# Kernel optimization log

Hardware: AMD Instinct MI355X
Metric: run time of the kernel (lower is better)

The kernel has to match this reference:

```python
import jax, jax.numpy as jnp
import numpy as np

D = 8        # q_ndim (= dof_ndim)
HID = 200    # hidden_size
N = 16384    # batch of states
EPS = 0.1    # qdot regularizer coefficient in L()


def _lagrangian(z, Ws, bs):
    # z: (2D,) = [q, qdot]; angular_dims=() so CosSin is an identity pass-through
    v = z[D:]
    h = z
    for W, b in zip(Ws[:-1], bs[:-1]):
        h = jax.nn.softplus(h @ W + b)   # FCsoftplus blocks
    L = (h @ Ws[-1] + bs[-1])[0]          # final Linear -> scalar (Reshape(-1))
    return L + EPS * jnp.dot(v, v)


def setup_inputs():
    key = jax.random.key(0)
    ks = jax.random.split(key, 5)
    z = jax.random.normal(ks[0], (N, 2 * D), dtype=jnp.float32)
    t = jnp.zeros((), dtype=jnp.float32)

    def lin(k, fi, fo, scale):
        return (jax.random.normal(k, (fi, fo), dtype=jnp.float32)
                * jnp.float32(scale / np.sqrt(fi)))

    W0 = lin(ks[1], 2 * D, HID, 1.0)
    W1 = lin(ks[2], HID, HID, 1.0)
    W2 = lin(ks[3], HID, HID, 1.0)
    W3 = lin(ks[4], HID, 1, 0.01)  # small head keeps mass matrix M well conditioned
    b0 = jnp.zeros((HID,), jnp.float32)  # zero_bias init per FCsoftplus/Linear
    b1 = jnp.zeros((HID,), jnp.float32)
    b2 = jnp.zeros((HID,), jnp.float32)
    b3 = jnp.zeros((1,), jnp.float32)
    return dict(t=t, z=z, W0=W0, b0=b0, W1=W1, b1=b1, W2=W2, b2=b2, W3=W3, b3=b3)


def reference(t, z, W0, b0, W1, b1, W2, b2, W3, b3):
    # Euler-Lagrange dynamics (LagrangianDynamics):
    #   M a = dL/dq - (d2L/dq dv) v,  M = d2L/dv2;  dz/dt = [v, a]
    Ws = (W0, W1, W2, W3)
    bs = (b0, b1, b2, b3)
    Lfn = lambda zz: _lagrangian(zz, Ws, bs)

    def dyn_single(zi):
        g = jax.grad(Lfn)(zi)              # (2D,)  = [dL/dq, dL/dv]
        H = jax.jacfwd(jax.grad(Lfn))(zi)  # (2D,2D) Hessian of L wrt z
        v = zi[D:]
        M = H[D:, D:]                      # d(dL/dv)/dv  -> mass matrix
        C = H[D:, :D]                      # d(dL/dv)/dq
        F = g[:D] - C @ v
        a = jnp.linalg.solve(M, F)
        return jnp.concatenate([v, a])     # (2D,)

    return jax.vmap(dyn_single)(z)         # (N, 2D)
```

## Files before the change

### kernel.cpp

```cpp
#include <hip/hip_runtime.h>
#include <math.h>

#define DD 8
#define ZD 16
#define HID 200
#define EPSL 0.1f
#define BS 16
#define NTHREADS 1024
#define NKC 7
#define NMT 13
#define XSTR 216
#define CSTR 212
#define HSTR 20
#define WSTR 208
#define NTAN 8
#define NT8 8

#define KSC 1024.0f
#define SSC 64.0f
#define INV_K (1.0f/1024.0f)
#define INV_KS (1.0f/65536.0f)

typedef _Float16 half8 __attribute__((ext_vector_type(8)));
typedef _Float16 half4v __attribute__((ext_vector_type(4)));
typedef _Float16 half2v __attribute__((ext_vector_type(2)));
typedef float float4v __attribute__((ext_vector_type(4)));

#define S4 (NKC*NMT*64*8)
#define OFF_W1T 0
#define OFF_W2T (S4)
#define OFF_W1  (2*S4)
#define OFF_W2  (3*S4)
#define OFF_W0T (4*S4)
#define OFF_W0  (4*S4 + NMT*64*8)
#define WS_HALFS (4*S4 + NMT*64*8 + NKC*64*8)

__global__ void prep(const float* __restrict__ W0, const float* __restrict__ W1,
                     const float* __restrict__ W2, _Float16* __restrict__ ws)
{
    int idx = blockIdx.x * 256 + threadIdx.x;
    if (idx >= WS_HALFS) return;
    float v = 0.f;
    if (idx < 4*S4) {
        int arr = idx / S4, e = idx % S4;
        int kc = e / (NMT*64*8); int r = e % (NMT*64*8);
        int mt = r / (64*8); r %= 64*8;
        int lane = r / 8, j = r % 8;
        int m = mt*16 + (lane & 15);
        int k = kc*32 + (lane >> 4)*8 + j;
        if (m < HID && k < HID) {
            if      (arr == 0) v = W1[k*HID + m];
            else if (arr == 1) v = W2[k*HID + m];
            else if (arr == 2) v = W1[m*HID + k];
            else               v = W2[m*HID + k];
        }
    } else if (idx < OFF_W0) {
        int e = idx - OFF_W0T;
        int mt = e / (64*8); int r = e % (64*8);
        int lane = r / 8, j = r % 8;
        int m = mt*16 + (lane & 15);
        int k = (lane >> 4)*8 + j;
        if (m < HID && k < ZD) v = W0[k*HID + m];
    } else {
        int e = idx - OFF_W0;
        int kc = e / (64*8); int r = e % (64*8);
        int lane = r / 8, j = r % 8;
        int m = (lane & 15);
        int k = kc*32 + (lane >> 4)*8 + j;
        if (k < HID) v = W0[m*HID + k];
    }
    ws[idx] = (_Float16)v;
}

__device__ __forceinline__ half4v pk4(float4v a) {
    half2v lo = __builtin_bit_cast(half2v, __builtin_amdgcn_cvt_pkrtz(a.x, a.y));
    half2v hi = __builtin_bit_cast(half2v, __builtin_amdgcn_cvt_pkrtz(a.z, a.w));
    return __builtin_shufflevector(lo, hi, 0, 1, 2, 3);
}
__device__ __forceinline__ void sig_sp(float x, float& sp, float& sg) {
    float e = __expf(-fabsf(x));
    float r = 1.0f / (1.0f + e);
    sg = (x >= 0.f) ? r : (1.0f - r);
    sp = fmaxf(x, 0.f) + __logf(1.f + e);
}

template<int NTILES, int MTC>
__device__ __forceinline__ void run_mv(const half8* __restrict__ Asw,
                                       const _Float16* __restrict__ Xsrc,
                                       int mt0, int lane,
                                       float4v acc[MTC][NTILES])
{
    const int lm = lane & 15, q = lane >> 4;
    constexpr int PF = (NTILES > 1) ? 2 : NKC;
#pragma unroll
    for (int m = 0; m < MTC; ++m)
#pragma unroll
        for (int n = 0; n < NTILES; ++n)
            acc[m][n] = (float4v){0.f, 0.f, 0.f, 0.f};

    half8 a[MTC][PF];
#pragma unroll
    for (int p = 0; p < PF; ++p)
#pragma unroll
        for (int m = 0; m < MTC; ++m)
            a[m][p] = Asw[(p*NMT + mt0 + m)*64 + lane];

#pragma unroll
    for (int kc = 0; kc < NKC; ++kc) {
        half8 x[NTILES];
#pragma unroll
        for (int n = 0; n < NTILES; ++n)
            x[n] = *(const half8*)(Xsrc + (n*16 + lm)*XSTR + kc*32 + q*8);
        half8 an[MTC];
        if (kc + PF < NKC)
#pragma unroll
            for (int m = 0; m < MTC; ++m)
                an[m] = Asw[((kc+PF)*NMT + mt0 + m)*64 + lane];
#pragma unroll
        for (int m = 0; m < MTC; ++m)
#pragma unroll
            for (int n = 0; n < NTILES; ++n)
                acc[m][n] = __builtin_amdgcn_mfma_f32_16x16x32_f16(a[m][0], x[n], acc[m][n], 0, 0, 0);
#pragma unroll
        for (int m = 0; m < MTC; ++m)
#pragma unroll
            for (int p = 0; p + 1 < PF; ++p) a[m][p] = a[m][p+1];
        if (kc + PF < NKC)
#pragma unroll
            for (int m = 0; m < MTC; ++m) a[m][PF-1] = an[m];
    }
}

__global__ void __launch_bounds__(NTHREADS, 4)
lnn_main(const float* __restrict__ z,
         const float* __restrict__ W0, const float* __restrict__ b0,
         const float* __restrict__ b1, const float* __restrict__ b2,
         const float* __restrict__ W3,
         const _Float16* __restrict__ ws,
         float* __restrict__ out)
{
    __shared__ alignas(16) _Float16 Xt[128*XSTR];
    __shared__ alignas(16) _Float16 Xb[128*XSTR];
    __shared__ alignas(16) _Float16 Cf[5][16*CSTR];
    __shared__ alignas(16) _Float16 Xz[16*40];
    __shared__ alignas(16) _Float16 bsh[4*WSTR];
    __shared__ alignas(16) _Float16 w0t[NTAN*WSTR];
    __shared__ alignas(16) float gsh[16*HSTR];
    __shared__ alignas(16) float Hr[128*HSTR];

    const int tid  = threadIdx.x;
    const int wave = tid >> 6;
    const int lane = tid & 63;
    const int lm   = lane & 15;
    const int q    = lane >> 4;
    const int s0   = blockIdx.x * BS;

    const half8* W1Tsw = (const half8*)(ws + OFF_W1T);
    const half8* W2Tsw = (const half8*)(ws + OFF_W2T);
    const half8* W1sw  = (const half8*)(ws + OFF_W1);
    const half8* W2sw  = (const half8*)(ws + OFF_W2);
    const half8* W0Tsw = (const half8*)(ws + OFF_W0T);
    const half8* W0sw  = (const half8*)(ws + OFF_W0);

    if (tid < 256) {
        int s = tid >> 4, k = tid & 15;
        Xz[s*40 + k]      = (_Float16)z[(s0 + s)*ZD + k];
        Xz[s*40 + 16 + k] = (_Float16)0.f;
    }
    for (int idx = tid; idx < 128*16; idx += NTHREADS) {
        int r = idx >> 4, c = 200 + (idx & 15);
        Xt[r*XSTR + c] = (_Float16)0.f;
        Xb[r*XSTR + c] = (_Float16)0.f;
    }
    if (tid < 8) {
        Xt[16*XSTR + tid] = (_Float16)0.f;
        Xb[16*XSTR + tid] = (_Float16)0.f;
    }
    for (int idx = tid; idx < 4*WSTR; idx += NTHREADS) {
        int l = idx / WSTR, u = idx % WSTR;
        float v = 0.f;
        if (u < HID) {
            if      (l == 0) v = b0[u];
            else if (l == 1) v = b1[u];
            else if (l == 2) v = b2[u];
            else             v = KSC * W3[u];
        }
        bsh[idx] = (_Float16)v;
    }
    for (int idx = tid; idx < NTAN*WSTR; idx += NTHREADS) {
        int t = idx / WSTR, u = idx % WSTR;
        w0t[idx] = (_Float16)((u < HID) ? SSC * W0[(DD + t)*HID + u] : 0.f);
    }
    __syncthreads();

    float4v acc1[1][1];
    const int ubf = wave*16 + q*4;

    if (wave < NMT) {
        acc1[0][0] = (float4v){0.f,0.f,0.f,0.f};
        half8 xz = *(const half8*)(Xz + lm*40 + q*8);
        half8 a = W0Tsw[wave*64 + lane];
        acc1[0][0] = __builtin_amdgcn_mfma_f32_16x16x32_f16(a, xz, acc1[0][0], 0, 0, 0);
        half4v bb = *(const half4v*)(&bsh[0*WSTR + ubf]);
        float h[4], p[4];
#pragma unroll
        for (int r = 0; r < 4; ++r) {
            float av = acc1[0][0][r] + (float)bb[r];
            sig_sp(av, h[r], p[r]);
        }
        *(half4v*)(&Xt[lm*XSTR + ubf])     = pk4((float4v){h[0],h[1],h[2],h[3]});
        *(half4v*)(&Cf[0][lm*CSTR + ubf])  = pk4((float4v){p[0],p[1],p[2],p[3]});
    }
    __syncthreads();

    if (wave < NMT) {
        run_mv<1,1>(W1Tsw, Xt, wave, lane, acc1);
        half4v bb = *(const half4v*)(&bsh[1*WSTR + ubf]);
        float h[4], p[4];
#pragma unroll
        for (int r = 0; r < 4; ++r) {
            float av = acc1[0][0][r] + (float)bb[r];
            sig_sp(av, h[r], p[r]);
        }
        *(half4v*)(&Xb[lm*XSTR + ubf])    = pk4((float4v){h[0],h[1],h[2],h[3]});
        *(half4v*)(&Cf[1][lm*CSTR + ubf]) = pk4((float4v){p[0],p[1],p[2],p[3]});
    }
    __syncthreads();

    if (wave < NMT) {
        run_mv<1,1>(W2Tsw, Xb, wave, lane, acc1);
        half4v bb = *(const half4v*)(&bsh[2*WSTR + ubf]);
        half4v w3 = *(const half4v*)(&bsh[3*WSTR + ubf]);
        float d2[4], c2[4];
#pragma unroll
        for (int r = 0; r < 4; ++r) {
            float av = acc1[0][0][r] + (float)bb[r];
            float e = __expf(-fabsf(av));
            float rr = 1.f / (1.f + e);
            float sg = (av >= 0.f) ? rr : (1.f - rr);
            float wk = (float)w3[r];
            d2[r] = wk * sg;
            c2[r] = wk * sg * (1.f - sg);
        }
        *(half4v*)(&Xt[lm*XSTR + ubf])    = pk4((float4v){d2[0],d2[1],d2[2],d2[3]});
        *(half4v*)(&Cf[2][lm*CSTR + ubf]) = pk4((float4v){c2[0],c2[1],c2[2],c2[3]});
    }
    __syncthreads();

    if (wave < NMT) {
        run_mv<1,1>(W2sw, Xt, wave, lane, acc1);
        half4v p1 = *(const half4v*)(&Cf[1][lm*CSTR + ubf]);
        half4v u1 = pk4(acc1[0][0]);
        half4v one = {(_Float16)1.f,(_Float16)1.f,(_Float16)1.f,(_Float16)1.f};
        *(half4v*)(&Xb[lm*XSTR + ubf])    = u1 * p1;
        *(half4v*)(&Cf[3][lm*CSTR + ubf]) = u1 * (one - p1);
    }
    __syncthreads();

    if (wave < NMT) {
        run_mv<1,1>(W1sw, Xb, wave, lane, acc1);
        half4v p0 = *(const half4v*)(&Cf[0][lm*CSTR + ubf]);
        half4v u0 = pk4(acc1[0][0]);
        half4v one = {(_Float16)1.f,(_Float16)1.f,(_Float16)1.f,(_Float16)1.f};
        half4v d0 = u0 * p0;
        *(half4v*)(&Xt[lm*XSTR + ubf])    = d0;
        *(half4v*)(&Cf[4][lm*CSTR + ubf]) = d0 * (one - p0);
    }
    __syncthreads();

    if (wave == 0) {
        half8 aw[NKC];
#pragma unroll
        for (int kc = 0; kc < NKC; ++kc) aw[kc] = W0sw[kc*64 + lane];
        float4v g = (float4v){0.f,0.f,0.f,0.f};
#pragma unroll
        for (int kc = 0; kc < NKC; ++kc) {
            half8 x = *(const half8*)(Xt + lm*XSTR + kc*32 + q*8);
            g = __builtin_amdgcn_mfma_f32_16x16x32_f16(aw[kc], x, g, 0, 0, 0);
        }
        float4v gv; gv.x = g.x*INV_K; gv.y = g.y*INV_K; gv.z = g.z*INV_K; gv.w = g.w*INV_K;
        *(float4v*)(&gsh[lm*HSTR + q*4]) = gv;
    } else {
        for (int idx = tid - 64; idx < 128*50; idx += NTHREADS - 64) {
            int row = idx / 50, u = (idx % 50)*4;
            int s = row & 15, t = row >> 4;
            half4v p0 = *(const half4v*)(&Cf[0][s*CSTR + u]);
            half4v w0 = *(const half4v*)(&w0t[t*WSTR + u]);
            *(half4v*)(&Xb[row*XSTR + u]) = p0 * w0;
        }
    }
    __syncthreads();

    float4v acc8[1][NT8];
    half4v c3th1[NT8];

    if (wave < NMT) {
        run_mv<NT8,1>(W1Tsw, Xb, wave, lane, acc8);
        half4v p1 = *(const half4v*)(&Cf[1][lm*CSTR + ubf]);
        half4v c3 = *(const half4v*)(&Cf[3][lm*CSTR + ubf]);
#pragma unroll
        for (int n = 0; n < NT8; ++n) {
            half4v t = pk4(acc8[0][n]) * p1;
            *(half4v*)(&Xt[(n*16 + lm)*XSTR + ubf]) = t;
            c3th1[n] = c3 * t;
        }
    }
    __syncthreads();

    if (wave < NMT) {
        run_mv<NT8,1>(W2Tsw, Xt, wave, lane, acc8);
        half4v c2 = *(const half4v*)(&Cf[2][lm*CSTR + ubf]);
#pragma unroll
        for (int n = 0; n < NT8; ++n)
            *(half4v*)(&Xb[(n*16 + lm)*XSTR + ubf]) = pk4(acc8[0][n]) * c2;
    }
    __syncthreads();

    if (wave < NMT) {
        run_mv<NT8,1>(W2sw, Xb, wave, lane, acc8);
        half4v p1 = *(const half4v*)(&Cf[1][lm*CSTR + ubf]);
#pragma unroll
        for (int n = 0; n < NT8; ++n)
            *(half4v*)(&Xt[(n*16 + lm)*XSTR + ubf]) = pk4(acc8[0][n]) * p1 + c3th1[n];
    }
    __syncthreads();

    if (wave < NMT) {
        run_mv<NT8,1>(W1sw, Xt, wave, lane, acc8);
        half4v p0 = *(const half4v*)(&Cf[0][lm*CSTR + ubf]);
        half4v c4 = *(const half4v*)(&Cf[4][lm*CSTR + ubf]);
#pragma unroll
        for (int n = 0; n < NT8; ++n) {
            half4v w0 = *(const half4v*)(&w0t[n*WSTR + ubf]);
            *(half4v*)(&Xb[(n*16 + lm)*XSTR + ubf]) = pk4(acc8[0][n]) * p0 + c4 * w0;
        }
    }
    __syncthreads();

    if (wave < 8) {
        half8 aw[NKC];
#pragma unroll
        for (int kc = 0; kc < NKC; ++kc) aw[kc] = W0sw[kc*64 + lane];
        float4v hacc = (float4v){0.f,0.f,0.f,0.f};
#pragma unroll
        for (int kc = 0; kc < NKC; ++kc) {
            half8 x = *(const half8*)(Xb + (wave*16 + lm)*XSTR + kc*32 + q*8);
            hacc = __builtin_amdgcn_mfma_f32_16x16x32_f16(aw[kc], x, hacc, 0, 0, 0);
        }
        int row = wave*16 + lm;
        float4v hv;
        hv.x = hacc.x*INV_KS; hv.y = hacc.y*INV_KS;
        hv.z = hacc.z*INV_KS; hv.w = hacc.w*INV_KS;
        *(float4v*)(&Hr[row*HSTR + q*4]) = hv;
    }
    __syncthreads();

    if (tid < BS) {
        const int s = tid;
        float M[DD][DD], F[DD], v[DD], a[DD];
#pragma unroll
        for (int c = 0; c < DD; ++c) v[c] = z[(s0 + s)*ZD + DD + c];
#pragma unroll
        for (int r = 0; r < DD; ++r) {
            float f = gsh[s*HSTR + r];
#pragma unroll
            for (int c = 0; c < DD; ++c) {
                M[r][c] = Hr[(r*16 + s)*HSTR + DD + c] + ((r == c) ? 2.f*EPSL : 0.f);
                f -= Hr[(r*16 + s)*HSTR + c] * v[c];
            }
            F[r] = f;
        }
#pragma unroll
        for (int col = 0; col < DD; ++col) {
            const float inv = 1.f / M[col][col];
#pragma unroll
            for (int r = col + 1; r < DD; ++r) {
                const float fac = M[r][col] * inv;
#pragma unroll
                for (int c = col + 1; c < DD; ++c) M[r][c] -= fac * M[col][c];
                F[r] -= fac * F[col];
            }
        }
#pragma unroll
        for (int r = DD - 1; r >= 0; --r) {
            float ssum = F[r];
#pragma unroll
            for (int c = r + 1; c < DD; ++c) ssum -= M[r][c] * a[c];
            a[r] = ssum / M[r][r];
        }
        float* op = out + (size_t)(s0 + s)*ZD;
#pragma unroll
        for (int c = 0; c < DD; ++c) { op[c] = v[c]; op[DD + c] = a[c]; }
    }
}

extern "C" void kernel_launch(void* const* d_in, const int* in_sizes, int n_in,
                              void* d_out, int out_size, void* d_ws, size_t ws_size,
                              hipStream_t stream)
{
    const float* z  = (const float*)d_in[1];
    const float* W0 = (const float*)d_in[2];
    const float* b0 = (const float*)d_in[3];
    const float* W1 = (const float*)d_in[4];
    const float* b1 = (const float*)d_in[5];
    const float* W2 = (const float*)d_in[6];
    const float* b2 = (const float*)d_in[7];
    const float* W3 = (const float*)d_in[8];
    float* out = (float*)d_out;
    _Float16* ws = (_Float16*)d_ws;

    const int n = in_sizes[1] / (2*DD);

    prep<<<dim3((WS_HALFS + 255)/256), dim3(256), 0, stream>>>(W0, W1, W2, ws);
    lnn_main<<<dim3(n / BS), dim3(NTHREADS), 0, stream>>>(
        z, W0, b0, b1, b2, W3, ws, out);
}
```

Before: 172.4 us.

## Halve block to 8 samples and 512 threads with two M-tiles per wave

Cuts the batch per block from 16 to 8 samples and the block from 1024 to 512 threads. The 13 output M-tiles are redistributed so waves 0-4 each handle two tiles and waves 5-7 handle one, so all eight waves do work. The tangent phase drops from 8 to 4 N-tiles, and LDS buffers shrink with tighter strides, which should allow more resident blocks and less idle waves. In exchange the first-phase MFMAs run on 16-row tiles that hold only 8 real samples, so half of that compute is wasted. The reduced strides may also add LDS bank conflicts, and there is now padding and masking logic for the partial last tile.

After: 166.9 us. 3.2% less time.

```diff
diff --git a/kernel.cpp b/kernel.cpp
--- a/kernel.cpp
+++ b/kernel.cpp
@@ -5,16 +5,15 @@
 #define ZD 16
 #define HID 200
 #define EPSL 0.1f
-#define BS 16
-#define NTHREADS 1024
+#define BS 8
+#define NTHREADS 512
 #define NKC 7
 #define NMT 13
-#define XSTR 216
-#define CSTR 212
-#define HSTR 20
+#define XSTR 200
+#define CSTR 208
 #define WSTR 208
 #define NTAN 8
-#define NT8 8
+#define NT4 4
 
 #define KSC 1024.0f
 #define SSC 64.0f
@@ -139,14 +138,14 @@
          const _Float16* __restrict__ ws,
          float* __restrict__ out)
 {
-    __shared__ alignas(16) _Float16 Xt[128*XSTR];
-    __shared__ alignas(16) _Float16 Xb[128*XSTR];
-    __shared__ alignas(16) _Float16 Cf[5][16*CSTR];
-    __shared__ alignas(16) _Float16 Xz[16*40];
+    __shared__ alignas(16) _Float16 Xt[64*XSTR + 24];
+    __shared__ alignas(16) _Float16 Xb[64*XSTR + 24];
+    __shared__ alignas(16) _Float16 Cf[5][8*CSTR];
+    __shared__ alignas(16) _Float16 Xz[16*32];
     __shared__ alignas(16) _Float16 bsh[4*WSTR];
     __shared__ alignas(16) _Float16 w0t[NTAN*WSTR];
-    __shared__ alignas(16) float gsh[16*HSTR];
-    __shared__ alignas(16) float Hr[128*HSTR];
+    __shared__ alignas(16) float gsh[8*16];
+    __shared__ alignas(16) float Hr[64*16];
 
     const int tid  = threadIdx.x;
     const int wave = tid >> 6;
@@ -155,6 +154,9 @@
     const int q    = lane >> 4;
     const int s0   = blockIdx.x * BS;
 
+    const int mt0 = (wave < 5) ? wave*2 : (10 + (wave - 5));
+    const int mtc = (wave < 5) ? 2 : 1;
+
     const half8* W1Tsw = (const half8*)(ws + OFF_W1T);
     const half8* W2Tsw = (const half8*)(ws + OFF_W2T);
     const half8* W1sw  = (const half8*)(ws + OFF_W1);
@@ -162,19 +164,15 @@
     const half8* W0Tsw = (const half8*)(ws + OFF_W0T);
     const half8* W0sw  = (const half8*)(ws + OFF_W0);
 
-    if (tid < 256) {
-        int s = tid >> 4, k = tid & 15;
-        Xz[s*40 + k]      = (_Float16)z[(s0 + s)*ZD + k];
-        Xz[s*40 + 16 + k] = (_Float16)0.f;
-    }
-    for (int idx = tid; idx < 128*16; idx += NTHREADS) {
-        int r = idx >> 4, c = 200 + (idx & 15);
-        Xt[r*XSTR + c] = (_Float16)0.f;
-        Xb[r*XSTR + c] = (_Float16)0.f;
-    }
-    if (tid < 8) {
+    for (int idx = tid; idx < 16*32; idx += NTHREADS) {
+        int s = idx >> 5, c = idx & 31;
+        Xz[idx] = (s < BS && c < ZD) ? (_Float16)z[(s0 + s)*ZD + c] : (_Float16)0.f;
+    }
+    if (tid < 24) {
         Xt[16*XSTR + tid] = (_Float16)0.f;
         Xb[16*XSTR + tid] = (_Float16)0.f;
+        Xt[64*XSTR + tid] = (_Float16)0.f;
+        Xb[64*XSTR + tid] = (_Float16)0.f;
     }
     for (int idx = tid; idx < 4*WSTR; idx += NTHREADS) {
         int l = idx / WSTR, u = idx % WSTR;
@@ -193,78 +191,111 @@
     }
     __syncthreads();
 
-    float4v acc1[1][1];
-    const int ubf = wave*16 + q*4;
-
-    if (wave < NMT) {
-        acc1[0][0] = (float4v){0.f,0.f,0.f,0.f};
-        half8 xz = *(const half8*)(Xz + lm*40 + q*8);
-        half8 a = W0Tsw[wave*64 + lane];
-        acc1[0][0] = __builtin_amdgcn_mfma_f32_16x16x32_f16(a, xz, acc1[0][0], 0, 0, 0);
-        half4v bb = *(const half4v*)(&bsh[0*WSTR + ubf]);
-        float h[4], p[4];
-#pragma unroll
-        for (int r = 0; r < 4; ++r) {
-            float av = acc1[0][0][r] + (float)bb[r];
-            sig_sp(av, h[r], p[r]);
-        }
-        *(half4v*)(&Xt[lm*XSTR + ubf])     = pk4((float4v){h[0],h[1],h[2],h[3]});
-        *(half4v*)(&Cf[0][lm*CSTR + ubf])  = pk4((float4v){p[0],p[1],p[2],p[3]});
-    }
-    __syncthreads();
-
-    if (wave < NMT) {
-        run_mv<1,1>(W1Tsw, Xt, wave, lane, acc1);
-        half4v bb = *(const half4v*)(&bsh[1*WSTR + ubf]);
-        float h[4], p[4];
-#pragma unroll
-        for (int r = 0; r < 4; ++r) {
-            float av = acc1[0][0][r] + (float)bb[r];
-            sig_sp(av, h[r], p[r]);
-        }
-        *(half4v*)(&Xb[lm*XSTR + ubf])    = pk4((float4v){h[0],h[1],h[2],h[3]});
-        *(half4v*)(&Cf[1][lm*CSTR + ubf]) = pk4((float4v){p[0],p[1],p[2],p[3]});
-    }
-    __syncthreads();
-
-    if (wave < NMT) {
-        run_mv<1,1>(W2Tsw, Xb, wave, lane, acc1);
-        half4v bb = *(const half4v*)(&bsh[2*WSTR + ubf]);
-        half4v w3 = *(const half4v*)(&bsh[3*WSTR + ubf]);
-        float d2[4], c2[4];
-#pragma unroll
-        for (int r = 0; r < 4; ++r) {
-            float av = acc1[0][0][r] + (float)bb[r];
-            float e = __expf(-fabsf(av));
-            float rr = 1.f / (1.f + e);
-            float sg = (av >= 0.f) ? rr : (1.f - rr);
-            float wk = (float)w3[r];
-            d2[r] = wk * sg;
-            c2[r] = wk * sg * (1.f - sg);
-        }
-        *(half4v*)(&Xt[lm*XSTR + ubf])    = pk4((float4v){d2[0],d2[1],d2[2],d2[3]});
-        *(half4v*)(&Cf[2][lm*CSTR + ubf]) = pk4((float4v){c2[0],c2[1],c2[2],c2[3]});
-    }
-    __syncthreads();
-
-    if (wave < NMT) {
-        run_mv<1,1>(W2sw, Xt, wave, lane, acc1);
-        half4v p1 = *(const half4v*)(&Cf[1][lm*CSTR + ubf]);
-        half4v u1 = pk4(acc1[0][0]);
-        half4v one = {(_Float16)1.f,(_Float16)1.f,(_Float16)1.f,(_Float16)1.f};
-        *(half4v*)(&Xb[lm*XSTR + ubf])    = u1 * p1;
-        *(half4v*)(&Cf[3][lm*CSTR + ubf]) = u1 * (one - p1);
-    }
-    __syncthreads();
-
-    if (wave < NMT) {
-        run_mv<1,1>(W1sw, Xb, wave, lane, acc1);
-        half4v p0 = *(const half4v*)(&Cf[0][lm*CSTR + ubf]);
-        half4v u0 = pk4(acc1[0][0]);
-        half4v one = {(_Float16)1.f,(_Float16)1.f,(_Float16)1.f,(_Float16)1.f};
-        half4v d0 = u0 * p0;
-        *(half4v*)(&Xt[lm*XSTR + ubf])    = d0;
-        *(half4v*)(&Cf[4][lm*CSTR + ubf]) = d0 * (one - p0);
+    float4v acc1[2][1];
+
+    {
+        half8 xz = *(const half8*)(Xz + lm*32 + q*8);
+#pragma unroll
+        for (int m = 0; m < 2; ++m)
+            if (m < mtc) {
+                acc1[m][0] = (float4v){0.f,0.f,0.f,0.f};
+                half8 a = W0Tsw[(mt0 + m)*64 + lane];
+                acc1[m][0] = __builtin_amdgcn_mfma_f32_16x16x32_f16(a, xz, acc1[m][0], 0, 0, 0);
+                const int ub = (mt0 + m)*16 + q*4;
+                const bool padq = (mt0 + m == 12) && (q >= 2);
+                half4v bb = *(const half4v*)(&bsh[0*WSTR + ub]);
+                float h[4], p[4];
+#pragma unroll
+                for (int r = 0; r < 4; ++r) {
+                    float av = acc1[m][0][r] + (float)bb[r];
+                    sig_sp(av, h[r], p[r]);
+                }
+                if (!padq) *(half4v*)(&Xt[lm*XSTR + ub]) = pk4((float4v){h[0],h[1],h[2],h[3]});
+                if (lm < BS) *(half4v*)(&Cf[0][lm*CSTR + ub]) = pk4((float4v){p[0],p[1],p[2],p[3]});
+            }
+    }
+    __syncthreads();
+
+    {
+        if (mtc == 2) run_mv<1,2>(W1Tsw, Xt, mt0, lane, acc1);
+        else          run_mv<1,1>(W1Tsw, Xt, mt0, lane, acc1);
+#pragma unroll
+        for (int m = 0; m < 2; ++m)
+            if (m < mtc) {
+                const int ub = (mt0 + m)*16 + q*4;
+                const bool padq = (mt0 + m == 12) && (q >= 2);
+                half4v bb = *(const half4v*)(&bsh[1*WSTR + ub]);
+                float h[4], p[4];
+#pragma unroll
+                for (int r = 0; r < 4; ++r) {
+                    float av = acc1[m][0][r] + (float)bb[r];
+                    sig_sp(av, h[r], p[r]);
+                }
+                if (!padq) *(half4v*)(&Xb[lm*XSTR + ub]) = pk4((float4v){h[0],h[1],h[2],h[3]});
+                if (lm < BS) *(half4v*)(&Cf[1][lm*CSTR + ub]) = pk4((float4v){p[0],p[1],p[2],p[3]});
+            }
+    }
+    __syncthreads();
+
+    {
+        if (mtc == 2) run_mv<1,2>(W2Tsw, Xb, mt0, lane, acc1);
+        else          run_mv<1,1>(W2Tsw, Xb, mt0, lane, acc1);
+#pragma unroll
+        for (int m = 0; m < 2; ++m)
+            if (m < mtc) {
+                const int ub = (mt0 + m)*16 + q*4;
+                const bool padq = (mt0 + m == 12) && (q >= 2);
+                half4v bb = *(const half4v*)(&bsh[2*WSTR + ub]);
+                half4v w3 = *(const half4v*)(&bsh[3*WSTR + ub]);
+                float d2[4], c2[4];
+#pragma unroll
+                for (int r = 0; r < 4; ++r) {
+                    float av = acc1[m][0][r] + (float)bb[r];
+                    float e = __expf(-fabsf(av));
+                    float rr = 1.f / (1.f + e);
+                    float sg = (av >= 0.f) ? rr : (1.f - rr);
+                    float wk = (float)w3[r];
+                    d2[r] = wk * sg;
+                    c2[r] = wk * sg * (1.f - sg);
+                }
+                if (!padq) *(half4v*)(&Xt[lm*XSTR + ub]) = pk4((float4v){d2[0],d2[1],d2[2],d2[3]});
+                if (lm < BS) *(half4v*)(&Cf[2][lm*CSTR + ub]) = pk4((float4v){c2[0],c2[1],c2[2],c2[3]});
+            }
+    }
+    __syncthreads();
+
+    {
+        if (mtc == 2) run_mv<1,2>(W2sw, Xt, mt0, lane, acc1);
+        else          run_mv<1,1>(W2sw, Xt, mt0, lane, acc1);
+#pragma unroll
+        for (int m = 0; m < 2; ++m)
+            if (m < mtc) {
+                const int ub = (mt0 + m)*16 + q*4;
+                const bool padq = (mt0 + m == 12) && (q >= 2);
+                half4v p1 = *(const half4v*)(&Cf[1][(lm & 7)*CSTR + ub]);
+                half4v u1 = pk4(acc1[m][0]);
+                half4v one = {(_Float16)1.f,(_Float16)1.f,(_Float16)1.f,(_Float16)1.f};
+                if (!padq) *(half4v*)(&Xb[lm*XSTR + ub]) = u1 * p1;
+                if (lm < BS) *(half4v*)(&Cf[3][lm*CSTR + ub]) = u1 * (one - p1);
+            }
+    }
+    __syncthreads();
+
+    {
+        if (mtc == 2) run_mv<1,2>(W1sw, Xb, mt0, lane, acc1);
+        else          run_mv<1,1>(W1sw, Xb, mt0, lane, acc1);
+#pragma unroll
+        for (int m = 0; m < 2; ++m)
+            if (m < mtc) {
+                const int ub = (mt0 + m)*16 + q*4;
+                const bool padq = (mt0 + m == 12) && (q >= 2);
+                half4v p0 = *(const half4v*)(&Cf[0][(lm & 7)*CSTR + ub]);
+                half4v u0 = pk4(acc1[m][0]);
+                half4v one = {(_Float16)1.f,(_Float16)1.f,(_Float16)1.f,(_Float16)1.f};
+                half4v d0 = u0 * p0;
+                if (!padq) *(half4v*)(&Xt[lm*XSTR + ub]) = d0;
+                if (lm < BS) *(half4v*)(&Cf[4][lm*CSTR + ub]) = d0 * (one - p0);
+            }
     }
     __syncthreads();
 
@@ -278,12 +309,14 @@
             half8 x = *(const half8*)(Xt + lm*XSTR + kc*32 + q*8);
             g = __builtin_amdgcn_mfma_f32_16x16x32_f16(aw[kc], x, g, 0, 0, 0);
         }
-        float4v gv; gv.x = g.x*INV_K; gv.y = g.y*INV_K; gv.z = g.z*INV_K; gv.w = g.w*INV_K;
-        *(float4v*)(&gsh[lm*HSTR + q*4]) = gv;
+        if (lm < BS) {
+            float4v gv; gv.x = g.x*INV_K; gv.y = g.y*INV_K; gv.z = g.z*INV_K; gv.w = g.w*INV_K;
+            *(float4v*)(&gsh[lm*16 + q*4]) = gv;
+        }
     } else {
-        for (int idx = tid - 64; idx < 128*50; idx += NTHREADS - 64) {
+        for (int idx = tid - 64; idx < 64*50; idx += NTHREADS - 64) {
             int row = idx / 50, u = (idx % 50)*4;
-            int s = row & 15, t = row >> 4;
+            int s = row & 7, t = row >> 3;
             half4v p0 = *(const half4v*)(&Cf[0][s*CSTR + u]);
             half4v w0 = *(const half4v*)(&w0t[t*WSTR + u]);
             *(half4v*)(&Xb[row*XSTR + u]) = p0 * w0;
@@ -291,53 +324,82 @@
     }
     __syncthreads();
 
-    float4v acc8[1][NT8];
-    half4v c3th1[NT8];
-
-    if (wave < NMT) {
-        run_mv<NT8,1>(W1Tsw, Xb, wave, lane, acc8);
-        half4v p1 = *(const half4v*)(&Cf[1][lm*CSTR + ubf]);
-        half4v c3 = *(const half4v*)(&Cf[3][lm*CSTR + ubf]);
-#pragma unroll
-        for (int n = 0; n < NT8; ++n) {
-            half4v t = pk4(acc8[0][n]) * p1;
-            *(half4v*)(&Xt[(n*16 + lm)*XSTR + ubf]) = t;
-            c3th1[n] = c3 * t;
-        }
-    }
-    __syncthreads();
-
-    if (wave < NMT) {
-        run_mv<NT8,1>(W2Tsw, Xt, wave, lane, acc8);
-        half4v c2 = *(const half4v*)(&Cf[2][lm*CSTR + ubf]);
-#pragma unroll
-        for (int n = 0; n < NT8; ++n)
-            *(half4v*)(&Xb[(n*16 + lm)*XSTR + ubf]) = pk4(acc8[0][n]) * c2;
-    }
-    __syncthreads();
-
-    if (wave < NMT) {
-        run_mv<NT8,1>(W2sw, Xb, wave, lane, acc8);
-        half4v p1 = *(const half4v*)(&Cf[1][lm*CSTR + ubf]);
-#pragma unroll
-        for (int n = 0; n < NT8; ++n)
-            *(half4v*)(&Xt[(n*16 + lm)*XSTR + ubf]) = pk4(acc8[0][n]) * p1 + c3th1[n];
-    }
-    __syncthreads();
-
-    if (wave < NMT) {
-        run_mv<NT8,1>(W1sw, Xt, wave, lane, acc8);
-        half4v p0 = *(const half4v*)(&Cf[0][lm*CSTR + ubf]);
-        half4v c4 = *(const half4v*)(&Cf[4][lm*CSTR + ubf]);
-#pragma unroll
-        for (int n = 0; n < NT8; ++n) {
-            half4v w0 = *(const half4v*)(&w0t[n*WSTR + ubf]);
-            *(half4v*)(&Xb[(n*16 + lm)*XSTR + ubf]) = pk4(acc8[0][n]) * p0 + c4 * w0;
-        }
-    }
-    __syncthreads();
-
-    if (wave < 8) {
+    float4v acc4[2][NT4];
+    half4v c3th1[2][NT4];
+
+    {
+        if (mtc == 2) run_mv<NT4,2>(W1Tsw, Xb, mt0, lane, acc4);
+        else          run_mv<NT4,1>(W1Tsw, Xb, mt0, lane, acc4);
+#pragma unroll
+        for (int m = 0; m < 2; ++m)
+            if (m < mtc) {
+                const int ub = (mt0 + m)*16 + q*4;
+                const bool padq = (mt0 + m == 12) && (q >= 2);
+                half4v p1 = *(const half4v*)(&Cf[1][(lm & 7)*CSTR + ub]);
+                half4v c3 = *(const half4v*)(&Cf[3][(lm & 7)*CSTR + ub]);
+#pragma unroll
+                for (int n = 0; n < NT4; ++n) {
+                    half4v t = pk4(acc4[m][n]) * p1;
+                    if (!padq) *(half4v*)(&Xt[(n*16 + lm)*XSTR + ub]) = t;
+                    c3th1[m][n] = c3 * t;
+                }
+            }
+    }
+    __syncthreads();
+
+    {
+        if (mtc == 2) run_mv<NT4,2>(W2Tsw, Xt, mt0, lane, acc4);
+        else          run_mv<NT4,1>(W2Tsw, Xt, mt0, lane, acc4);
+#pragma unroll
+        for (int m = 0; m < 2; ++m)
+            if (m < mtc) {
+                const int ub = (mt0 + m)*16 + q*4;
+                const bool padq = (mt0 + m == 12) && (q >= 2);
+                half4v c2 = *(const half4v*)(&Cf[2][(lm & 7)*CSTR + ub]);
+#pragma unroll
+                for (int n = 0; n < NT4; ++n)
+                    if (!padq) *(half4v*)(&Xb[(n*16 + lm)*XSTR + ub]) = pk4(acc4[m][n]) * c2;
+            }
+    }
+    __syncthreads();
+
+    {
+        if (mtc == 2) run_mv<NT4,2>(W2sw, Xb, mt0, lane, acc4);
+        else          run_mv<NT4,1>(W2sw, Xb, mt0, lane, acc4);
+#pragma unroll
+        for (int m = 0; m < 2; ++m)
+            if (m < mtc) {
+                const int ub = (mt0 + m)*16 + q*4;
+                const bool padq = (mt0 + m == 12) && (q >= 2);
+                half4v p1 = *(const half4v*)(&Cf[1][(lm & 7)*CSTR + ub]);
+#pragma unroll
+                for (int n = 0; n < NT4; ++n)
+                    if (!padq) *(half4v*)(&Xt[(n*16 + lm)*XSTR + ub]) = pk4(acc4[m][n]) * p1 + c3th1[m][n];
+            }
+    }
+    __syncthreads();
+
+    {
+        if (mtc == 2) run_mv<NT4,2>(W1sw, Xt, mt0, lane, acc4);
+        else          run_mv<NT4,1>(W1sw, Xt, mt0, lane, acc4);
+#pragma unroll
+        for (int m = 0; m < 2; ++m)
+            if (m < mtc) {
+                const int ub = (mt0 + m)*16 + q*4;
+                const bool padq = (mt0 + m == 12) && (q >= 2);
+                half4v p0 = *(const half4v*)(&Cf[0][(lm & 7)*CSTR + ub]);
+                half4v c4 = *(const half4v*)(&Cf[4][(lm & 7)*CSTR + ub]);
+#pragma unroll
+                for (int n = 0; n < NT4; ++n) {
+                    int t = n*2 + (lm >> 3);
+                    half4v w0 = *(const half4v*)(&w0t[t*WSTR + ub]);
+                    if (!padq) *(half4v*)(&Xb[(n*16 + lm)*XSTR + ub]) = pk4(acc4[m][n]) * p0 + c4 * w0;
+                }
+            }
+    }
+    __syncthreads();
+
+    if (wave < 4) {
         half8 aw[NKC];
 #pragma unroll
         for (int kc = 0; kc < NKC; ++kc) aw[kc] = W0sw[kc*64 + lane];
@@ -351,7 +413,7 @@
         float4v hv;
         hv.x = hacc.x*INV_KS; hv.y = hacc.y*INV_KS;
         hv.z = hacc.z*INV_KS; hv.w = hacc.w*INV_KS;
-        *(float4v*)(&Hr[row*HSTR + q*4]) = hv;
+        *(float4v*)(&Hr[row*16 + q*4]) = hv;
     }
     __syncthreads();
 
@@ -362,11 +424,11 @@
         for (int c = 0; c < DD; ++c) v[c] = z[(s0 + s)*ZD + DD + c];
 #pragma unroll
         for (int r = 0; r < DD; ++r) {
-            float f = gsh[s*HSTR + r];
+            float f = gsh[s*16 + r];
 #pragma unroll
             for (int c = 0; c < DD; ++c) {
-                M[r][c] = Hr[(r*16 + s)*HSTR + DD + c] + ((r == c) ? 2.f*EPSL : 0.f);
-                f -= Hr[(r*16 + s)*HSTR + c] * v[c];
+                M[r][c] = Hr[(r*8 + s)*16 + DD + c] + ((r == c) ? 2.f*EPSL : 0.f);
+                f -= Hr[(r*8 + s)*16 + c] * v[c];
             }
             F[r] = f;
         }
```
